# Optimization experiments

Measured on AMD Instinct MI355X. Metric: run time of the kernel, lower is better.

Reference implementation:

```python
import jax, jax.numpy as jnp
import numpy as np

M, N = 256, 65536          # matched masks, flattened pred-mask pixels (256x256)
BLOCK_AREA = 4.0           # (H_t*W_t)/N with target masks at 512x512
H_T = W_T = 512.0
NUM_MASKS = 256.0
MAX_ITERS = 20
TOL = 1e-7


def _eval_fS(z, lam, Kcol):
    p = jax.nn.sigmoid(z + lam)
    f = jnp.sum(p, axis=-1, keepdims=True) - Kcol
    s = jnp.sum(p * (1.0 - p), axis=-1, keepdims=True)
    return f, s


def _shift_core(z, K):
    # z: (M,1,N) logits, K: (M,1) target counts. Safeguarded Newton/bisection
    # so that sum(sigmoid(z + lam)) == K per row. (torch ref uses float64;
    # we stay in input dtype for jit/bf16 compatibility.)
    n = z.shape[-1]
    K = jnp.clip(K, 0.0, float(n))
    z_max = jnp.max(z, axis=-1, keepdims=True)
    z_min = jnp.min(z, axis=-1, keepdims=True)
    L = -20.0 - z_max
    U = 20.0 - z_min

    def _logit(x, eps=1e-6):
        x = jnp.clip(x, eps, 1.0 - eps)
        return jnp.log(x) - jnp.log1p(-x)

    p0_mean = jnp.mean(jax.nn.sigmoid(z), axis=-1)
    t_mean = K / n
    lam = (_logit(t_mean) - _logit(p0_mean))[..., None]
    lam = jnp.clip(lam, L, U)
    Kcol = K[..., None]
    f, S = _eval_fS(z, lam, Kcol)

    def body(_, carry):
        lam, f, S, L, U = carry
        done = jnp.abs(f) <= TOL
        newton = lam - f / (S + 1e-18)
        oob = (newton < L) | (newton > U)
        lam_try = jnp.where(oob | done, lam, newton)
        f_try, _ = _eval_fS(z, lam_try, Kcol)
        no_improve = (jnp.abs(f_try) > jnp.abs(f)) & (~oob) & (~done)
        mid = 0.5 * (L + U)
        lam_next = jnp.where(oob | no_improve, mid, lam_try)
        f_next, S_next = _eval_fS(z, lam_next, Kcol)
        go_upper = f_next > 0
        U = jnp.where(go_upper, lam_next, U)
        L = jnp.where(go_upper, L, lam_next)
        return lam_next, f_next, S_next, L, U

    lam, f, S, L, U = jax.lax.fori_loop(0, MAX_ITERS, body, (lam, f, S, L, U))
    lam = jnp.clip(lam, L, U)
    return z + lam


def setup_inputs() -> dict:
    key = jax.random.key(0)
    k1, k2 = jax.random.split(key)
    logits = jax.random.normal(k1, (M, N), dtype=jnp.float32) * 2.0
    pos_counts = jax.random.uniform(k2, (M, N), dtype=jnp.float32) * BLOCK_AREA
    return {"logits": logits, "pos_counts": pos_counts}


def reference(logits, pos_counts):
    n = logits.shape[1]
    K_high = jnp.sum(pos_counts, axis=1)                      # (M,)
    K_low = jnp.clip(K_high / BLOCK_AREA, 0.0, float(n))      # (M,)
    z_shift = _shift_core(logits[:, None, :], K_low[:, None])[:, 0, :]
    # block-weighted BCE with logits (numerically stable form)
    abs_z = jnp.abs(z_shift)
    max_z = jnp.maximum(z_shift, 0.0)
    logexp = jnp.log1p(jnp.exp(-abs_z))
    loss_block = BLOCK_AREA * max_z - z_shift * pos_counts + BLOCK_AREA * logexp
    loss_mask = jnp.sum(jnp.sum(loss_block, axis=1) / (H_T * W_T)) / NUM_MASKS
    # dice on area-matched probabilities
    probs = jax.nn.sigmoid(z_shift)
    inter = jnp.sum(probs * pos_counts, axis=1)
    pred_sum = BLOCK_AREA * jnp.sum(probs, axis=1)
    loss_dice = jnp.sum(1.0 - (2.0 * inter + 1.0) / (pred_sum + K_high + 1.0)) / NUM_MASKS
    return jnp.stack([loss_mask, loss_dice])
```

## Files before the change

kernel.cpp:

```cpp
#include <hip/hip_runtime.h>
#include <math.h>

#define NCOLS 65536
#define MROWS 256
#define NBINS 512
#define CHUNKS 16
#define CELEMS (NCOLS / CHUNKS)
#define K1_TPB 256
#define ZLO 20.0f
#define INVW ((float)NBINS / (2.0f * ZLO))
#define BINW (2.0f * ZLO / (float)NBINS)
#define PSCALE 32.0f
#define CNT_SHIFT 20
#define POS_MASK ((1u << CNT_SHIFT) - 1u)

#define GL16(gsrc, ldst) __builtin_amdgcn_global_load_lds(                    \
    (const __attribute__((address_space(1))) void*)(gsrc),                    \
    (__attribute__((address_space(3))) void*)(ldst), 16, 0, 0)

__device__ __forceinline__ float waveReduceSum(float v) {
#pragma unroll
  for (int off = 32; off > 0; off >>= 1) v += __shfl_xor(v, off, 64);
  return v;
}

__global__ __launch_bounds__(K1_TPB) void hist_kernel(
    const float* __restrict__ logits, const float* __restrict__ pos,
    unsigned int* __restrict__ gh) {
  __shared__ __align__(16) float zb[CELEMS];
  __shared__ __align__(16) float pb[CELEMS];
  __shared__ unsigned int h[NBINS];
  const int blk = blockIdx.x;
  const int row = blk / CHUNKS, chunk = blk % CHUNKS;
  const int tid = threadIdx.x;
  const int wv = tid >> 6, ln = tid & 63;

  h[tid] = 0u;
  h[tid + K1_TPB] = 0u;

  const float* zsrc = logits + (size_t)row * NCOLS + (size_t)chunk * CELEMS;
  const float* psrc = pos + (size_t)row * NCOLS + (size_t)chunk * CELEMS;

#pragma unroll
  for (int s = 0; s < 4; ++s) {
    const int off = wv * 1024 + s * 256;
    GL16(zsrc + off + ln * 4, &zb[off]);
    GL16(psrc + off + ln * 4, &pb[off]);
  }
  asm volatile("s_waitcnt vmcnt(0)" ::: "memory");
  __syncthreads();

#pragma unroll
  for (int s = 0; s < 4; ++s) {
    const int off = wv * 1024 + s * 256 + ln * 4;
    const float4 zv = *(const float4*)&zb[off];
    const float4 pv = *(const float4*)&pb[off];
    float zz[4] = {zv.x, zv.y, zv.z, zv.w};
    float pp[4] = {pv.x, pv.y, pv.z, pv.w};
#pragma unroll
    for (int c = 0; c < 4; ++c) {
      int b = (int)((zz[c] + ZLO) * INVW);
      b = min(max(b, 0), NBINS - 1);
      unsigned int pk = (1u << CNT_SHIFT) |
                        (unsigned int)__float2int_rn(pp[c] * PSCALE);
      atomicAdd(&h[b], pk);
    }
  }
  __syncthreads();
  const size_t base = (size_t)blk * NBINS;
  gh[base + tid] = h[tid];
  gh[base + tid + K1_TPB] = h[tid + K1_TPB];
}

#define K2_TPB 256

__global__ __launch_bounds__(K2_TPB) void solve_kernel(
    const unsigned int* __restrict__ gh, float* __restrict__ rowout) {
  __shared__ float cs[NBINS], ps[NBINS];
  const int row = blockIdx.x;
  const int tid = threadIdx.x;

#pragma unroll
  for (int j = 0; j < NBINS / K2_TPB; ++j) {
    const int b = tid + j * K2_TPB;
    unsigned int c = 0u, q = 0u;
    const size_t base = (size_t)row * CHUNKS * NBINS + b;
#pragma unroll
    for (int ch = 0; ch < CHUNKS; ++ch) {
      const unsigned int v = gh[base + (size_t)ch * NBINS];
      c += v >> CNT_SHIFT;
      q += v & POS_MASK;
    }
    cs[b] = (float)c;
    ps[b] = (float)q * (1.0f / PSCALE);
  }
  __syncthreads();
  if (tid >= 64) return;

  const int lane = tid;
  float cnt[8], pb[8], zc[8];
  float Kh = 0.0f, Szp = 0.0f;
#pragma unroll
  for (int j = 0; j < 8; ++j) {
    const int b = lane + 64 * j;
    cnt[j] = cs[b];
    pb[j] = ps[b];
    zc[j] = -ZLO + ((float)b + 0.5f) * BINW;
    Kh += pb[j];
    Szp += zc[j] * pb[j];
  }
  Kh = waveReduceSum(Kh);
  Szp = waveReduceSum(Szp);
  const float K = fminf(fmaxf(Kh * 0.25f, 0.0f), (float)NCOLS);

  float Lb = -2.0f * ZLO, Ub = 2.0f * ZLO, lam = 0.0f;
  for (int it = 0; it < 40; ++it) {
    float fp = 0.0f, sp = 0.0f;
#pragma unroll
    for (int j = 0; j < 8; ++j) {
      const float p = 1.0f / (1.0f + __expf(-(zc[j] + lam)));
      fp += cnt[j] * p;
      sp += cnt[j] * p * (1.0f - p);
    }
    fp = waveReduceSum(fp);
    sp = waveReduceSum(sp);
    const float f = fp - K;
    if (fabsf(f) <= 1e-2f) break;
    if (f > 0.0f) Ub = lam; else Lb = lam;
    const float newton = lam - f / (sp + 1e-12f);
    lam = (newton > Lb && newton < Ub) ? newton : 0.5f * (Lb + Ub);
  }

  float tl = 0.0f, ti = 0.0f, tp = 0.0f;
#pragma unroll
  for (int j = 0; j < 8; ++j) {
    const float zs = zc[j] + lam;
    const float e = __expf(-fabsf(zs));
    const float lg = __logf(1.0f + e);
    const float mz = fmaxf(zs, 0.0f);
    const float sig = (zs >= 0.0f) ? (1.0f / (1.0f + e)) : (e / (1.0f + e));
    tl += cnt[j] * (mz + lg);
    ti += pb[j] * sig;
    tp += cnt[j] * sig;
  }
  tl = waveReduceSum(tl);
  ti = waveReduceSum(ti);
  tp = waveReduceSum(tp);
  if (lane == 0) {
    float* o = rowout + row * 4;
    o[0] = 4.0f * tl - (Szp + lam * Kh);
    o[1] = ti;
    o[2] = tp;
    o[3] = Kh;
  }
}

__global__ void final_kernel(const float* __restrict__ rowout, float* __restrict__ out) {
  const int t = threadIdx.x;
  const float loss = rowout[t * 4 + 0];
  const float inter = rowout[t * 4 + 1];
  const float psum = rowout[t * 4 + 2];
  const float Kh = rowout[t * 4 + 3];
  float maskc = loss * (1.0f / (512.0f * 512.0f));
  float dicec = 1.0f - (2.0f * inter + 1.0f) / (4.0f * psum + Kh + 1.0f);
  maskc = waveReduceSum(maskc);
  dicec = waveReduceSum(dicec);
  __shared__ float red[8];
  const int wid = t >> 6, lane = t & 63;
  if (lane == 0) { red[wid] = maskc; red[4 + wid] = dicec; }
  __syncthreads();
  if (t == 0) {
    float a = 0.0f, b = 0.0f;
    for (int j = 0; j < 4; ++j) { a += red[j]; b += red[4 + j]; }
    out[0] = a / 256.0f;
    out[1] = b / 256.0f;
  }
}

#define FB_TPB 1024
#define FB_NV4 (NCOLS / 4 / FB_TPB)
__device__ __forceinline__ void fbReduce2(float a, float b, float* red,
                                          int wid, int lane, float& A, float& B) {
  a = waveReduceSum(a);
  b = waveReduceSum(b);
  __syncthreads();
  if (lane == 0) { red[wid] = a; red[16 + wid] = b; }
  __syncthreads();
  float ta = 0.0f, tb = 0.0f;
#pragma unroll
  for (int j = 0; j < 16; ++j) { ta += red[j]; tb += red[16 + j]; }
  A = ta; B = tb;
}

__global__ __launch_bounds__(FB_TPB) void fb_row_kernel(
    const float* __restrict__ logits, const float* __restrict__ pos,
    float* __restrict__ rowout) {
  __shared__ unsigned int h_cnt[2048];
  __shared__ int h_sum[2048];
  __shared__ float red[64];
  const int row = blockIdx.x;
  const int tid = threadIdx.x, wid = tid >> 6, lane = tid & 63;
  const float4* z4 = (const float4*)(logits + (size_t)row * NCOLS);
  const float4* p4 = (const float4*)(pos + (size_t)row * NCOLS);
  for (int b = tid; b < 2048; b += FB_TPB) { h_cnt[b] = 0u; h_sum[b] = 0; }
  __syncthreads();
  const float invw = 2048.0f / 40.0f;
  float s_pos = 0.0f;
#pragma unroll
  for (int i = 0; i < FB_NV4; ++i) {
    float4 zv = z4[i * FB_TPB + tid];
    float4 pv = p4[i * FB_TPB + tid];
    s_pos += (pv.x + pv.y) + (pv.z + pv.w);
    float zz[4] = {zv.x, zv.y, zv.z, zv.w};
#pragma unroll
    for (int c = 0; c < 4; ++c) {
      int b = (int)((zz[c] + 20.0f) * invw);
      b = min(max(b, 0), 2047);
      atomicAdd(&h_cnt[b], 1u);
      atomicAdd(&h_sum[b], __float2int_rn(zz[c] * 1024.0f));
    }
  }
  float K_high, dummy;
  fbReduce2(s_pos, 0.0f, red, wid, lane, K_high, dummy);
  float K = fminf(fmaxf(K_high * 0.25f, 0.0f), (float)NCOLS);
  const float c0 = (float)h_cnt[tid];
  const float c1 = (float)h_cnt[tid + FB_TPB];
  const float zb0 = (c0 > 0.0f) ? (float)h_sum[tid] / (1024.0f * c0) : 0.0f;
  const float zb1 = (c1 > 0.0f) ? (float)h_sum[tid + FB_TPB] / (1024.0f * c1) : 0.0f;
  float Lb = -40.0f, Ub = 40.0f, lam = 0.0f;
  for (int it = 0; it < 40; ++it) {
    float p0 = 1.0f / (1.0f + __expf(-(zb0 + lam)));
    float p1 = 1.0f / (1.0f + __expf(-(zb1 + lam)));
    float F, S;
    fbReduce2(c0 * p0 + c1 * p1, c0 * p0 * (1.0f - p0) + c1 * p1 * (1.0f - p1),
              red, wid, lane, F, S);
    float f = F - K;
    if (fabsf(f) <= 1e-3f) break;
    if (f > 0.0f) Ub = lam; else Lb = lam;
    float newton = lam - f / (S + 1e-12f);
    lam = (newton > Lb && newton < Ub) ? newton : 0.5f * (Lb + Ub);
  }
  float loss = 0.0f, inter = 0.0f, psum = 0.0f;
#pragma unroll
  for (int i = 0; i < FB_NV4; ++i) {
    float4 zv = z4[i * FB_TPB + tid];
    float4 pv = p4[i * FB_TPB + tid];
    float zz[4] = {zv.x, zv.y, zv.z, zv.w};
    float pp[4] = {pv.x, pv.y, pv.z, pv.w};
#pragma unroll
    for (int c = 0; c < 4; ++c) {
      float zs = zz[c] + lam;
      float q = __expf(-fabsf(zs));
      loss += 4.0f * fmaxf(zs, 0.0f) - zs * pp[c] + 4.0f * __logf(1.0f + q);
      float sig = (zs >= 0.0f) ? (1.0f / (1.0f + q)) : (q / (1.0f + q));
      inter += sig * pp[c];
      psum += sig;
    }
  }
  float TL, TI;
  fbReduce2(loss, inter, red, wid, lane, TL, TI);
  float TP, d2;
  fbReduce2(psum, 0.0f, red, wid, lane, TP, d2);
  if (tid == 0) {
    float* o = rowout + row * 4;
    o[0] = TL; o[1] = TI; o[2] = TP; o[3] = K_high;
  }
}

extern "C" void kernel_launch(void* const* d_in, const int* in_sizes, int n_in,
                              void* d_out, int out_size, void* d_ws, size_t ws_size,
                              hipStream_t stream) {
  const float* logits = (const float*)d_in[0];
  const float* pos = (const float*)d_in[1];
  char* ws = (char*)d_ws;

  const size_t nblk = (size_t)MROWS * CHUNKS;
  const size_t off_gh = 0;
  const size_t off_rowout = off_gh + nblk * NBINS * sizeof(unsigned int);
  const size_t needed = off_rowout + (size_t)MROWS * 4 * sizeof(float);

  if (ws_size >= needed) {
    unsigned int* gh = (unsigned int*)(ws + off_gh);
    float* rowout = (float*)(ws + off_rowout);
    hist_kernel<<<(int)nblk, K1_TPB, 0, stream>>>(logits, pos, gh);
    solve_kernel<<<MROWS, K2_TPB, 0, stream>>>(gh, rowout);
    final_kernel<<<1, 256, 0, stream>>>(rowout, (float*)d_out);
  } else {
    float* rowout = (float*)d_ws;
    fb_row_kernel<<<MROWS, FB_TPB, 0, stream>>>(logits, pos, rowout);
    final_kernel<<<1, 256, 0, stream>>>(rowout, (float*)d_out);
  }
}
```

Before: 32.78 us.

## Double-buffer LDS staging in histogram kernel with fewer, larger blocks per row

The histogram kernel now gives each block 16K elements, four blocks per row instead of sixteen. It streams them in 2K sub-chunks through double-buffered LDS, so async global-to-LDS loads of the next sub-chunk overlap with the shared-memory atomics on the current one. This cuts the number of partial histograms the solve kernel must merge, and the per-block histogram clear and write-out overhead. To fit larger per-block counts in the packed 32-bit bins, the count field shift and the pos quantisation scale are reduced. That coarsens the pos-weight precision and leaves less headroom against overflow in heavily populated bins.

```diff
diff --git a/kernel.cpp b/kernel.cpp
--- a/kernel.cpp
+++ b/kernel.cpp
@@ -4,14 +4,16 @@
 #define NCOLS 65536
 #define MROWS 256
 #define NBINS 512
-#define CHUNKS 16
-#define CELEMS (NCOLS / CHUNKS)
+#define SUBE 2048
+#define NSUB 8
+#define BLKE (SUBE * NSUB)
+#define BPR (NCOLS / BLKE)
 #define K1_TPB 256
 #define ZLO 20.0f
 #define INVW ((float)NBINS / (2.0f * ZLO))
 #define BINW (2.0f * ZLO / (float)NBINS)
-#define PSCALE 32.0f
-#define CNT_SHIFT 20
+#define PSCALE 8.0f
+#define CNT_SHIFT 19
 #define POS_MASK ((1u << CNT_SHIFT) - 1u)
 
 #define GL16(gsrc, ldst) __builtin_amdgcn_global_load_lds(                    \
@@ -27,49 +29,67 @@
 __global__ __launch_bounds__(K1_TPB) void hist_kernel(
     const float* __restrict__ logits, const float* __restrict__ pos,
     unsigned int* __restrict__ gh) {
-  __shared__ __align__(16) float zb[CELEMS];
-  __shared__ __align__(16) float pb[CELEMS];
+  __shared__ __align__(16) float zb[2][SUBE];
+  __shared__ __align__(16) float pb[2][SUBE];
   __shared__ unsigned int h[NBINS];
   const int blk = blockIdx.x;
-  const int row = blk / CHUNKS, chunk = blk % CHUNKS;
+  const int row = blk / BPR, seg = blk % BPR;
   const int tid = threadIdx.x;
   const int wv = tid >> 6, ln = tid & 63;
+  const int wq = wv * 512;
 
   h[tid] = 0u;
   h[tid + K1_TPB] = 0u;
 
-  const float* zsrc = logits + (size_t)row * NCOLS + (size_t)chunk * CELEMS;
-  const float* psrc = pos + (size_t)row * NCOLS + (size_t)chunk * CELEMS;
-
-#pragma unroll
-  for (int s = 0; s < 4; ++s) {
-    const int off = wv * 1024 + s * 256;
-    GL16(zsrc + off + ln * 4, &zb[off]);
-    GL16(psrc + off + ln * 4, &pb[off]);
-  }
-  asm volatile("s_waitcnt vmcnt(0)" ::: "memory");
-  __syncthreads();
-
-#pragma unroll
-  for (int s = 0; s < 4; ++s) {
-    const int off = wv * 1024 + s * 256 + ln * 4;
-    const float4 zv = *(const float4*)&zb[off];
-    const float4 pv = *(const float4*)&pb[off];
-    float zz[4] = {zv.x, zv.y, zv.z, zv.w};
-    float pp[4] = {pv.x, pv.y, pv.z, pv.w};
-#pragma unroll
-    for (int c = 0; c < 4; ++c) {
-      int b = (int)((zz[c] + ZLO) * INVW);
-      b = min(max(b, 0), NBINS - 1);
-      unsigned int pk = (1u << CNT_SHIFT) |
-                        (unsigned int)__float2int_rn(pp[c] * PSCALE);
-      atomicAdd(&h[b], pk);
-    }
+  const float* zs = logits + (size_t)row * NCOLS + (size_t)seg * BLKE;
+  const float* ps = pos + (size_t)row * NCOLS + (size_t)seg * BLKE;
+
+#define STAGE(par, c) do {                                                    \
+    const float* zsrc_ = zs + (c) * SUBE + wq;                                \
+    const float* psrc_ = ps + (c) * SUBE + wq;                                \
+    GL16(zsrc_ + ln * 4, &zb[par][wq]);                                       \
+    GL16(zsrc_ + 256 + ln * 4, &zb[par][wq + 256]);                           \
+    GL16(psrc_ + ln * 4, &pb[par][wq]);                                       \
+    GL16(psrc_ + 256 + ln * 4, &pb[par][wq + 256]);                           \
+  } while (0)
+
+#define PROC(par) do {                                                        \
+    _Pragma("unroll")                                                         \
+    for (int s2 = 0; s2 < 2; ++s2) {                                          \
+      const float4 zv = *(const float4*)&zb[par][wq + s2 * 256 + ln * 4];     \
+      const float4 pv = *(const float4*)&pb[par][wq + s2 * 256 + ln * 4];     \
+      float zz[4] = {zv.x, zv.y, zv.z, zv.w};                                 \
+      float pp[4] = {pv.x, pv.y, pv.z, pv.w};                                 \
+      _Pragma("unroll")                                                       \
+      for (int c4 = 0; c4 < 4; ++c4) {                                        \
+        int b = (int)((zz[c4] + ZLO) * INVW);                                 \
+        b = min(max(b, 0), NBINS - 1);                                        \
+        unsigned int pk = (1u << CNT_SHIFT) |                                 \
+                          (unsigned int)__float2int_rn(pp[c4] * PSCALE);      \
+        atomicAdd(&h[b], pk);                                                 \
+      }                                                                       \
+    }                                                                         \
+  } while (0)
+
+  STAGE(0, 0);
+  __syncthreads();
+
+  for (int c = 0; c < NSUB; ++c) {
+    if (c + 1 < NSUB) {
+      STAGE((c + 1) & 1, c + 1);
+      asm volatile("s_waitcnt vmcnt(4)" ::: "memory");
+    } else {
+      asm volatile("s_waitcnt vmcnt(0)" ::: "memory");
+    }
+    __builtin_amdgcn_sched_barrier(0);
+    PROC(c & 1);
   }
   __syncthreads();
   const size_t base = (size_t)blk * NBINS;
   gh[base + tid] = h[tid];
   gh[base + tid + K1_TPB] = h[tid + K1_TPB];
+#undef STAGE
+#undef PROC
 }
 
 #define K2_TPB 256
@@ -84,9 +104,9 @@
   for (int j = 0; j < NBINS / K2_TPB; ++j) {
     const int b = tid + j * K2_TPB;
     unsigned int c = 0u, q = 0u;
-    const size_t base = (size_t)row * CHUNKS * NBINS + b;
-#pragma unroll
-    for (int ch = 0; ch < CHUNKS; ++ch) {
+    const size_t base = (size_t)row * BPR * NBINS + b;
+#pragma unroll
+    for (int ch = 0; ch < BPR; ++ch) {
       const unsigned int v = gh[base + (size_t)ch * NBINS];
       c += v >> CNT_SHIFT;
       q += v & POS_MASK;
@@ -274,7 +294,7 @@
   const float* pos = (const float*)d_in[1];
   char* ws = (char*)d_ws;
 
-  const size_t nblk = (size_t)MROWS * CHUNKS;
+  const size_t nblk = (size_t)MROWS * BPR;
   const size_t off_gh = 0;
   const size_t off_rowout = off_gh + nblk * NBINS * sizeof(unsigned int);
   const size_t needed = off_rowout + (size_t)MROWS * 4 * sizeof(float);
```

Result: no change. 32.21 us (-1.7%).
